# Performance work log

Measured on AMD Instinct MI355X. Metric: run time of the kernel, lower is better.

Reference implementation:

```python
import jax, jax.numpy as jnp
import numpy as np
from jax import lax

N_NODES = 100000
N_EDGES = 3200000
IN_CH = 128
HID = 32
OUT_CH = 64
N_SG = 31  # conv1..conv31, each SGConv(32,32) with K=1 + relu


def setup_inputs() -> dict:
    key = jax.random.key(0)
    ks = jax.random.split(key, 8)
    x = jax.random.normal(ks[0], (N_NODES, IN_CH), dtype=jnp.float32)
    edge_index = jax.random.randint(ks[1], (2, N_EDGES), 0, N_NODES, dtype=jnp.int64)
    s0 = 1.0 / np.sqrt(IN_CH)
    sh = 1.0 / np.sqrt(HID)
    W0 = jax.random.uniform(ks[2], (IN_CH, HID), jnp.float32, -s0, s0)
    b0 = jnp.zeros((HID,), jnp.float32)
    Ws = jax.random.uniform(ks[3], (N_SG, HID, HID), jnp.float32, -sh, sh)
    bs = jnp.zeros((N_SG, HID), jnp.float32)
    W32 = jax.random.uniform(ks[4], (HID, OUT_CH), jnp.float32, -sh, sh)
    b32 = jnp.zeros((OUT_CH,), jnp.float32)
    return {"x": x, "W0": W0, "b0": b0, "Ws": Ws, "bs": bs,
            "W32": W32, "b32": b32, "edge_index": edge_index}


def reference(x, W0, b0, Ws, bs, W32, b32, edge_index):
    N = x.shape[0]
    # GCN normalization with added self-loops (PyG SGConv default, K=1)
    sl = jnp.arange(N, dtype=edge_index.dtype)
    row = jnp.concatenate([edge_index[0], sl])  # source nodes
    col = jnp.concatenate([edge_index[1], sl])  # destination nodes
    deg = jax.ops.segment_sum(jnp.ones(row.shape[0], x.dtype), col, num_segments=N)
    dinv = jnp.where(deg > 0, deg ** -0.5, 0.0)
    norm = dinv[row] * dinv[col]  # [E+N]

    h = x @ W0 + b0  # conv0: plain Linear -> [N, 32]

    def sg_layer(h, wb):
        W, b = wb
        # propagate: D^-1/2 (A+I) D^-1/2 h, then linear + relu
        agg = jax.ops.segment_sum(norm[:, None] * h[row], col, num_segments=N)
        return jax.nn.relu(agg @ W + b), None

    h, _ = lax.scan(sg_layer, h, (Ws, bs))  # conv1..conv31
    return h @ W32 + b32  # conv32: plain Linear -> [N, out_channels]
```

## Files before the change

kernel.cpp:

```cpp
#include <hip/hip_runtime.h>
#include <hip/hip_bf16.h>

#define THREADS 256
#define STRIDE 96

typedef _Float16 f16;
typedef f16 f16x8 __attribute__((ext_vector_type(8)));
typedef f16 f16x4 __attribute__((ext_vector_type(4)));


__global__ void fill_csr_range_kernel(const int* __restrict__ row, const int* __restrict__ col,
                                      int* __restrict__ fill, int* __restrict__ srcs,
                                      int E, int lo, int hi) {
    int e = blockIdx.x * blockDim.x + threadIdx.x;
    if (e < E) {
        int d = col[e];
        if (d >= lo && d < hi) {
            int c = atomicAdd(&fill[d], 1);
            if (c < STRIDE) srcs[(size_t)d * STRIDE + c] = row[e];
        }
    }
}

__global__ void pad_dinv_kernel(const int* __restrict__ fill, int* __restrict__ srcs,
                                float* __restrict__ dinv, int N) {
    int n = blockIdx.x * blockDim.x + threadIdx.x;
    if (n < N) {
        int d = min(fill[n], STRIDE);
        dinv[n] = 1.0f / sqrtf((float)(d + 1));
        int pd = (d + 7) & ~7;
        int* sp = srcs + (size_t)n * STRIDE;
        for (int j = d; j < pd; ++j) sp[j] = N;
    }
}

__global__ void zrow_kernel(f16* __restrict__ gA, f16* __restrict__ gB, int N) {
    int t = threadIdx.x;
    gA[(size_t)N * 32 + t] = (f16)0.f;
    gB[(size_t)N * 32 + t] = (f16)0.f;
}


__global__ __launch_bounds__(256) void lin0_kernel(const float* __restrict__ x,
        const float* __restrict__ W0, const float* __restrict__ b0,
        const float* __restrict__ dinv, f16* __restrict__ g, int N) {
    __shared__ float Ws[128 * 32];
    int t = threadIdx.x;
    for (int i = t; i < 128 * 32; i += 256) Ws[i] = W0[i];
    __syncthreads();
    int node = blockIdx.x * 32 + (t >> 3);
    int lane = t & 7;
    if (node >= N) return;
    float4 o = ((const float4*)b0)[lane];
    const float* xr = x + (size_t)node * 128;
    for (int k = 0; k < 128; ++k) {
        float a = xr[k];
        float4 w = *(const float4*)&Ws[k * 32 + lane * 4];
        o.x += a * w.x; o.y += a * w.y; o.z += a * w.z; o.w += a * w.w;
    }
    float di = dinv[node];
    f16x4 st;
    st.x = (f16)(o.x * di); st.y = (f16)(o.y * di);
    st.z = (f16)(o.z * di); st.w = (f16)(o.w * di);
    ((f16x4*)g)[(size_t)node * 8 + lane] = st;
}

__global__ __launch_bounds__(256, 6) void sg_layer_kernel(const f16* __restrict__ g_in,
        f16* __restrict__ g_out16, float* __restrict__ h_out32,
        const int* __restrict__ deg, const int* __restrict__ srcs,
        const float* __restrict__ dinv, const float* __restrict__ W,
        const float* __restrict__ b, int N, float bscale, int last) {
    __shared__ float Ws[32 * 32];
    int t = threadIdx.x;
    for (int i = t; i < 32 * 32; i += 256) Ws[i] = W[i];
    __syncthreads();
    int node = blockIdx.x * 64 + (t >> 2);
    int lane = t & 3;
    float o0=0.f,o1=0.f,o2=0.f,o3=0.f,o4=0.f,o5=0.f,o6=0.f,o7=0.f;
    if (node < N) {
        const f16x8* g8 = (const f16x8*)g_in;
        f16x8 sv = g8[(size_t)node * 4 + lane];
        o0=(float)sv[0]; o1=(float)sv[1]; o2=(float)sv[2]; o3=(float)sv[3];
        o4=(float)sv[4]; o5=(float)sv[5]; o6=(float)sv[6]; o7=(float)sv[7];
        int e = node * STRIDE;
        int e1 = e + ((min(deg[node], STRIDE) + 7) & ~7);
        int4 ia, ib;
        if (e < e1) {
            ia = *(const int4*)(srcs + e);
            ib = *(const int4*)(srcs + e + 4);
        }
        while (e < e1) {
            f16x8 v0 = g8[(size_t)ia.x * 4 + lane];
            f16x8 v1 = g8[(size_t)ia.y * 4 + lane];
            f16x8 v2 = g8[(size_t)ia.z * 4 + lane];
            f16x8 v3 = g8[(size_t)ia.w * 4 + lane];
            f16x8 v4 = g8[(size_t)ib.x * 4 + lane];
            f16x8 v5 = g8[(size_t)ib.y * 4 + lane];
            f16x8 v6 = g8[(size_t)ib.z * 4 + lane];
            f16x8 v7 = g8[(size_t)ib.w * 4 + lane];
            e += 8;
            if (e < e1) {
                ia = *(const int4*)(srcs + e);
                ib = *(const int4*)(srcs + e + 4);
            }
            o0 += (((float)v0[0]+(float)v1[0])+((float)v2[0]+(float)v3[0]))
                + (((float)v4[0]+(float)v5[0])+((float)v6[0]+(float)v7[0]));
            o1 += (((float)v0[1]+(float)v1[1])+((float)v2[1]+(float)v3[1]))
                + (((float)v4[1]+(float)v5[1])+((float)v6[1]+(float)v7[1]));
            o2 += (((float)v0[2]+(float)v1[2])+((float)v2[2]+(float)v3[2]))
                + (((float)v4[2]+(float)v5[2])+((float)v6[2]+(float)v7[2]));
            o3 += (((float)v0[3]+(float)v1[3])+((float)v2[3]+(float)v3[3]))
                + (((float)v4[3]+(float)v5[3])+((float)v6[3]+(float)v7[3]));
            o4 += (((float)v0[4]+(float)v1[4])+((float)v2[4]+(float)v3[4]))
                + (((float)v4[4]+(float)v5[4])+((float)v6[4]+(float)v7[4]));
            o5 += (((float)v0[5]+(float)v1[5])+((float)v2[5]+(float)v3[5]))
                + (((float)v4[5]+(float)v5[5])+((float)v6[5]+(float)v7[5]));
            o6 += (((float)v0[6]+(float)v1[6])+((float)v2[6]+(float)v3[6]))
                + (((float)v4[6]+(float)v5[6])+((float)v6[6]+(float)v7[6]));
            o7 += (((float)v0[7]+(float)v1[7])+((float)v2[7]+(float)v3[7]))
                + (((float)v4[7]+(float)v5[7])+((float)v6[7]+(float)v7[7]));
        }
    }
    if (node < N) {
        int c = lane * 8;
        int base = t & ~3;
        float m0=0.f,m1=0.f,m2=0.f,m3=0.f,m4=0.f,m5=0.f,m6=0.f,m7=0.f;
        #pragma unroll
        for (int kk = 0; kk < 32; ++kk) {
            float ov;
            switch (kk & 7) {
                case 0: ov = o0; break; case 1: ov = o1; break;
                case 2: ov = o2; break; case 3: ov = o3; break;
                case 4: ov = o4; break; case 5: ov = o5; break;
                case 6: ov = o6; break; default: ov = o7; break;
            }
            float a = __shfl(ov, base | (kk >> 3), 64);
            const float4* wr = (const float4*)&Ws[kk * 32 + c];
            float4 w0 = wr[0], w1 = wr[1];
            m0 += a * w0.x; m1 += a * w0.y; m2 += a * w0.z; m3 += a * w0.w;
            m4 += a * w1.x; m5 += a * w1.y; m6 += a * w1.z; m7 += a * w1.w;
        }
        float di = dinv[node];
        float4 ba = *(const float4*)&b[c];
        float4 bb = *(const float4*)&b[c + 4];
        float r0 = fmaxf(fmaf(di, m0, bscale * ba.x), 0.f);
        float r1 = fmaxf(fmaf(di, m1, bscale * ba.y), 0.f);
        float r2 = fmaxf(fmaf(di, m2, bscale * ba.z), 0.f);
        float r3 = fmaxf(fmaf(di, m3, bscale * ba.w), 0.f);
        float r4 = fmaxf(fmaf(di, m4, bscale * bb.x), 0.f);
        float r5 = fmaxf(fmaf(di, m5, bscale * bb.y), 0.f);
        float r6 = fmaxf(fmaf(di, m6, bscale * bb.z), 0.f);
        float r7 = fmaxf(fmaf(di, m7, bscale * bb.w), 0.f);
        if (!last) {
            float sc = 2.0f * di;
            f16x8 st;
            st[0]=(f16)(r0*sc); st[1]=(f16)(r1*sc); st[2]=(f16)(r2*sc); st[3]=(f16)(r3*sc);
            st[4]=(f16)(r4*sc); st[5]=(f16)(r5*sc); st[6]=(f16)(r6*sc); st[7]=(f16)(r7*sc);
            ((f16x8*)g_out16)[(size_t)node * 4 + lane] = st;
        } else {
            const float inv = 1.0f / 1073741824.0f;
            float4 wa = make_float4(r0*inv, r1*inv, r2*inv, r3*inv);
            float4 wb = make_float4(r4*inv, r5*inv, r6*inv, r7*inv);
            float4* hp = (float4*)(h_out32 + (size_t)node * 32 + c);
            hp[0] = wa; hp[1] = wb;
        }
    }
}

__global__ __launch_bounds__(256) void linout_kernel(const float* __restrict__ h,
        const float* __restrict__ W32, const float* __restrict__ b32,
        float* __restrict__ out, int N) {
    __shared__ float Ws[32 * 64];
    int t = threadIdx.x;
    for (int i = t; i < 32 * 64; i += 256) Ws[i] = W32[i];
    __syncthreads();
    int node = blockIdx.x * 16 + (t >> 4);
    int lane = t & 15;
    if (node >= N) return;
    float4 o = ((const float4*)b32)[lane];
    const float* hr = h + (size_t)node * 32;
    for (int k = 0; k < 32; ++k) {
        float a = hr[k];
        float4 w = *(const float4*)&Ws[k * 64 + lane * 4];
        o.x += a * w.x; o.y += a * w.y; o.z += a * w.z; o.w += a * w.w;
    }
    ((float4*)out)[(size_t)node * 16 + lane] = o;
}


extern "C" void kernel_launch(void* const* d_in, const int* in_sizes, int n_in,
                              void* d_out, int out_size, void* d_ws, size_t ws_size,
                              hipStream_t stream) {
    const float* x     = (const float*)d_in[0];
    const float* W0    = (const float*)d_in[1];
    const float* b0    = (const float*)d_in[2];
    const float* Wsall = (const float*)d_in[3];
    const float* bsall = (const float*)d_in[4];
    const float* W32   = (const float*)d_in[5];
    const float* b32   = (const float*)d_in[6];
    const int*   ei    = (const int*)d_in[7];

    const int N   = in_sizes[0] / 128;
    const int E   = in_sizes[7] / 2;
    const int NSG = in_sizes[3] / (32 * 32);
    const int* erow = ei;
    const int* ecol = ei + E;

    char* ws = (char*)d_ws;
    size_t off = 0;
    auto alloc = [&](size_t bytes) { size_t p = off; off += (bytes + 255) & ~(size_t)255; return p; };
    size_t fillOff  = alloc((size_t)N * 4);
    size_t dinvOff  = alloc((size_t)N * 4);
    size_t srcsOff  = alloc(((size_t)N * STRIDE + 8) * 4);
    size_t gAOff    = alloc((size_t)(N + 1) * 32 * 2);
    size_t gBOff    = alloc((size_t)(N + 1) * 32 * 2);
    size_t hFOff    = alloc((size_t)N * 32 * 4);

    int*   fill   = (int*)(ws + fillOff);
    float* dinv   = (float*)(ws + dinvOff);
    int*   srcs   = (int*)(ws + srcsOff);
    f16*   gA     = (f16*)(ws + gAOff);
    f16*   gB     = (f16*)(ws + gBOff);
    float* hF     = (float*)(ws + hFOff);

    (void)hipMemsetAsync(ws + fillOff, 0, (size_t)N * 4, stream);

    const int egrid = (E + THREADS - 1) / THREADS;
    const int ngrid = (N + THREADS - 1) / THREADS;

    for (int p = 0; p < 4; ++p) {
        int lo = (int)(((long long)N * p) / 4);
        int hi = (int)(((long long)N * (p + 1)) / 4);
        fill_csr_range_kernel<<<egrid, THREADS, 0, stream>>>(erow, ecol, fill, srcs, E, lo, hi);
    }
    pad_dinv_kernel<<<ngrid, THREADS, 0, stream>>>(fill, srcs, dinv, N);
    zrow_kernel<<<1, 32, 0, stream>>>(gA, gB, N);

    lin0_kernel<<<(N + 31) / 32, 256, 0, stream>>>(x, W0, b0, dinv, gA, N);

    f16* cur = gA;
    f16* nxt = gB;
    for (int l = 0; l < NSG; ++l) {
        int last = (l == NSG - 1) ? 1 : 0;
        float bscale = (float)(1u << l);
        sg_layer_kernel<<<(N + 63) / 64, 256, 0, stream>>>(
            cur, nxt, hF, fill, srcs, dinv,
            Wsall + (size_t)l * 32 * 32, bsall + (size_t)l * 32, N, bscale, last);
        f16* tmp = cur; cur = nxt; nxt = tmp;
    }

    linout_kernel<<<(N + 15) / 16, 256, 0, stream>>>(hF, W32, b32, (float*)d_out, N);
}
```

Before: 1.591 ms.

## Sort nodes by degree and build compact remapped CSR for balanced layers

Adds a degree histogram, a prefix scan and a ranking pass that renumber nodes in descending-degree order. It then builds a compact padded CSR whose source indices are already remapped to the new ranks. Each SG layer runs in permuted order, so threads in a wavefront have similar neighbor counts, which should cut divergence and idle lanes in the gather loop. The index array also becomes dense instead of fixed-stride. The cost is several extra preprocessing kernels, an indirection in lin0 and linout, and permuted node ids that change the memory locality of gathered features.

```diff
diff --git a/kernel.cpp b/kernel.cpp
--- a/kernel.cpp
+++ b/kernel.cpp
@@ -7,6 +7,8 @@
 typedef _Float16 f16;
 typedef f16 f16x8 __attribute__((ext_vector_type(8)));
 typedef f16 f16x4 __attribute__((ext_vector_type(4)));
+
+__device__ __forceinline__ int padlen(int d) { return (min(d, STRIDE) + 7) & ~7; }
 
 
 __global__ void fill_csr_range_kernel(const int* __restrict__ row, const int* __restrict__ col,
@@ -22,16 +24,67 @@
     }
 }
 
-__global__ void pad_dinv_kernel(const int* __restrict__ fill, int* __restrict__ srcs,
-                                float* __restrict__ dinv, int N) {
+__global__ void hist_kernel(const int* __restrict__ fill, int* __restrict__ hist, int N) {
+    int n = blockIdx.x * blockDim.x + threadIdx.x;
+    if (n < N) atomicAdd(&hist[127 - min(fill[n], 127)], 1);
+}
+
+__global__ void scan_hist_kernel(const int* __restrict__ hist,
+                                 int* __restrict__ binoff, int* __restrict__ ebase) {
+    __shared__ int sn[128], se[128];
+    int t = threadIdx.x;
+    int deg = 127 - t;
+    int pd = (min(max(deg, 0), STRIDE) + 7) & ~7;
+    int vn = hist[t];
+    int ve = vn * pd;
+    sn[t] = vn; se[t] = ve;
+    __syncthreads();
+    for (int off = 1; off < 128; off <<= 1) {
+        int xn = (t >= off) ? sn[t - off] : 0;
+        int xe = (t >= off) ? se[t - off] : 0;
+        __syncthreads();
+        sn[t] += xn; se[t] += xe;
+        __syncthreads();
+    }
+    binoff[t] = sn[t] - vn;
+    ebase[t]  = se[t] - ve;
+}
+
+__global__ void rank_kernel(const int* __restrict__ fill, const int* __restrict__ binoff,
+                            const int* __restrict__ ebase, int* __restrict__ binfill,
+                            int* __restrict__ rank, int* __restrict__ order,
+                            int* __restrict__ rstart, int* __restrict__ plen,
+                            float* __restrict__ dinv2, int N) {
     int n = blockIdx.x * blockDim.x + threadIdx.x;
     if (n < N) {
-        int d = min(fill[n], STRIDE);
-        dinv[n] = 1.0f / sqrtf((float)(d + 1));
-        int pd = (d + 7) & ~7;
-        int* sp = srcs + (size_t)n * STRIDE;
-        for (int j = d; j < pd; ++j) sp[j] = N;
-    }
+        int d = fill[n];
+        int b = 127 - min(d, 127);
+        int i = atomicAdd(&binfill[b], 1);
+        int p = binoff[b] + i;
+        int pd = padlen(d);
+        rank[n] = p;
+        order[p] = n;
+        rstart[p] = ebase[b] + i * pd;
+        plen[p] = pd;
+        dinv2[p] = 1.0f / sqrtf((float)(min(d, STRIDE) + 1));
+    }
+}
+
+__global__ void remap_kernel(const int* __restrict__ srcs, const int* __restrict__ order,
+                             const int* __restrict__ rank, const int* __restrict__ fill,
+                             const int* __restrict__ rstart, const int* __restrict__ plen,
+                             int* __restrict__ srcs2, int N) {
+    int t = threadIdx.x;
+    int p = blockIdx.x * 32 + (t >> 3);
+    if (p >= N) return;
+    int lane = t & 7;
+    int n = order[p];
+    int d = min(fill[n], STRIDE);
+    int pd = plen[p];
+    const int* sp = srcs + (size_t)n * STRIDE;
+    int* dp = srcs2 + rstart[p];
+    for (int j = lane; j < pd; j += 8)
+        dp[j] = (j < d) ? rank[sp[j]] : N;
 }
 
 __global__ void zrow_kernel(f16* __restrict__ gA, f16* __restrict__ gB, int N) {
@@ -43,51 +96,54 @@
 
 __global__ __launch_bounds__(256) void lin0_kernel(const float* __restrict__ x,
         const float* __restrict__ W0, const float* __restrict__ b0,
-        const float* __restrict__ dinv, f16* __restrict__ g, int N) {
+        const int* __restrict__ order, const float* __restrict__ dinv2,
+        f16* __restrict__ g, int N) {
     __shared__ float Ws[128 * 32];
     int t = threadIdx.x;
     for (int i = t; i < 128 * 32; i += 256) Ws[i] = W0[i];
     __syncthreads();
-    int node = blockIdx.x * 32 + (t >> 3);
+    int p = blockIdx.x * 32 + (t >> 3);
     int lane = t & 7;
-    if (node >= N) return;
+    if (p >= N) return;
+    int n = order[p];
     float4 o = ((const float4*)b0)[lane];
-    const float* xr = x + (size_t)node * 128;
+    const float* xr = x + (size_t)n * 128;
     for (int k = 0; k < 128; ++k) {
         float a = xr[k];
         float4 w = *(const float4*)&Ws[k * 32 + lane * 4];
         o.x += a * w.x; o.y += a * w.y; o.z += a * w.z; o.w += a * w.w;
     }
-    float di = dinv[node];
+    float di = dinv2[p];
     f16x4 st;
     st.x = (f16)(o.x * di); st.y = (f16)(o.y * di);
     st.z = (f16)(o.z * di); st.w = (f16)(o.w * di);
-    ((f16x4*)g)[(size_t)node * 8 + lane] = st;
+    ((f16x4*)g)[(size_t)p * 8 + lane] = st;
 }
 
 __global__ __launch_bounds__(256, 6) void sg_layer_kernel(const f16* __restrict__ g_in,
         f16* __restrict__ g_out16, float* __restrict__ h_out32,
-        const int* __restrict__ deg, const int* __restrict__ srcs,
-        const float* __restrict__ dinv, const float* __restrict__ W,
-        const float* __restrict__ b, int N, float bscale, int last) {
+        const int* __restrict__ rstart, const int* __restrict__ plen,
+        const int* __restrict__ srcs2, const float* __restrict__ dinv2,
+        const float* __restrict__ W, const float* __restrict__ b,
+        int N, float bscale, int last) {
     __shared__ float Ws[32 * 32];
     int t = threadIdx.x;
     for (int i = t; i < 32 * 32; i += 256) Ws[i] = W[i];
     __syncthreads();
-    int node = blockIdx.x * 64 + (t >> 2);
+    int p = blockIdx.x * 64 + (t >> 2);
     int lane = t & 3;
     float o0=0.f,o1=0.f,o2=0.f,o3=0.f,o4=0.f,o5=0.f,o6=0.f,o7=0.f;
-    if (node < N) {
+    if (p < N) {
         const f16x8* g8 = (const f16x8*)g_in;
-        f16x8 sv = g8[(size_t)node * 4 + lane];
+        f16x8 sv = g8[(size_t)p * 4 + lane];
         o0=(float)sv[0]; o1=(float)sv[1]; o2=(float)sv[2]; o3=(float)sv[3];
         o4=(float)sv[4]; o5=(float)sv[5]; o6=(float)sv[6]; o7=(float)sv[7];
-        int e = node * STRIDE;
-        int e1 = e + ((min(deg[node], STRIDE) + 7) & ~7);
+        int e = rstart[p];
+        int e1 = e + plen[p];
         int4 ia, ib;
         if (e < e1) {
-            ia = *(const int4*)(srcs + e);
-            ib = *(const int4*)(srcs + e + 4);
+            ia = *(const int4*)(srcs2 + e);
+            ib = *(const int4*)(srcs2 + e + 4);
         }
         while (e < e1) {
             f16x8 v0 = g8[(size_t)ia.x * 4 + lane];
@@ -100,8 +156,8 @@
             f16x8 v7 = g8[(size_t)ib.w * 4 + lane];
             e += 8;
             if (e < e1) {
-                ia = *(const int4*)(srcs + e);
-                ib = *(const int4*)(srcs + e + 4);
+                ia = *(const int4*)(srcs2 + e);
+                ib = *(const int4*)(srcs2 + e + 4);
             }
             o0 += (((float)v0[0]+(float)v1[0])+((float)v2[0]+(float)v3[0]))
                 + (((float)v4[0]+(float)v5[0])+((float)v6[0]+(float)v7[0]));
@@ -121,7 +177,7 @@
                 + (((float)v4[7]+(float)v5[7])+((float)v6[7]+(float)v7[7]));
         }
     }
-    if (node < N) {
+    if (p < N) {
         int c = lane * 8;
         int base = t & ~3;
         float m0=0.f,m1=0.f,m2=0.f,m3=0.f,m4=0.f,m5=0.f,m6=0.f,m7=0.f;
@@ -140,7 +196,7 @@
             m0 += a * w0.x; m1 += a * w0.y; m2 += a * w0.z; m3 += a * w0.w;
             m4 += a * w1.x; m5 += a * w1.y; m6 += a * w1.z; m7 += a * w1.w;
         }
-        float di = dinv[node];
+        float di = dinv2[p];
         float4 ba = *(const float4*)&b[c];
         float4 bb = *(const float4*)&b[c + 4];
         float r0 = fmaxf(fmaf(di, m0, bscale * ba.x), 0.f);
@@ -156,12 +212,12 @@
             f16x8 st;
             st[0]=(f16)(r0*sc); st[1]=(f16)(r1*sc); st[2]=(f16)(r2*sc); st[3]=(f16)(r3*sc);
             st[4]=(f16)(r4*sc); st[5]=(f16)(r5*sc); st[6]=(f16)(r6*sc); st[7]=(f16)(r7*sc);
-            ((f16x8*)g_out16)[(size_t)node * 4 + lane] = st;
+            ((f16x8*)g_out16)[(size_t)p * 4 + lane] = st;
         } else {
             const float inv = 1.0f / 1073741824.0f;
             float4 wa = make_float4(r0*inv, r1*inv, r2*inv, r3*inv);
             float4 wb = make_float4(r4*inv, r5*inv, r6*inv, r7*inv);
-            float4* hp = (float4*)(h_out32 + (size_t)node * 32 + c);
+            float4* hp = (float4*)(h_out32 + (size_t)p * 32 + c);
             hp[0] = wa; hp[1] = wb;
         }
     }
@@ -169,7 +225,7 @@
 
 __global__ __launch_bounds__(256) void linout_kernel(const float* __restrict__ h,
         const float* __restrict__ W32, const float* __restrict__ b32,
-        float* __restrict__ out, int N) {
+        const int* __restrict__ rank, float* __restrict__ out, int N) {
     __shared__ float Ws[32 * 64];
     int t = threadIdx.x;
     for (int i = t; i < 32 * 64; i += 256) Ws[i] = W32[i];
@@ -177,8 +233,9 @@
     int node = blockIdx.x * 16 + (t >> 4);
     int lane = t & 15;
     if (node >= N) return;
+    int p = rank[node];
     float4 o = ((const float4*)b32)[lane];
-    const float* hr = h + (size_t)node * 32;
+    const float* hr = h + (size_t)p * 32;
     for (int k = 0; k < 32; ++k) {
         float a = hr[k];
         float4 w = *(const float4*)&Ws[k * 64 + lane * 4];
@@ -210,20 +267,38 @@
     size_t off = 0;
     auto alloc = [&](size_t bytes) { size_t p = off; off += (bytes + 255) & ~(size_t)255; return p; };
     size_t fillOff  = alloc((size_t)N * 4);
+    size_t histOff  = alloc(128 * 4);
+    size_t bfilOff  = alloc(128 * 4);
+    size_t binoOff  = alloc(128 * 4);
+    size_t ebasOff  = alloc(128 * 4);
+    size_t rankOff  = alloc((size_t)N * 4);
+    size_t ordOff   = alloc((size_t)N * 4);
+    size_t rstOff   = alloc((size_t)N * 4);
+    size_t plenOff  = alloc((size_t)N * 4);
     size_t dinvOff  = alloc((size_t)N * 4);
-    size_t srcsOff  = alloc(((size_t)N * STRIDE + 8) * 4);
+    size_t srcsOff  = alloc((size_t)N * STRIDE * 4);
+    size_t srcs2Off = alloc(((size_t)E + 8 * (size_t)N + 64) * 4);
     size_t gAOff    = alloc((size_t)(N + 1) * 32 * 2);
     size_t gBOff    = alloc((size_t)(N + 1) * 32 * 2);
     size_t hFOff    = alloc((size_t)N * 32 * 4);
 
     int*   fill   = (int*)(ws + fillOff);
-    float* dinv   = (float*)(ws + dinvOff);
+    int*   hist   = (int*)(ws + histOff);
+    int*   bfil   = (int*)(ws + bfilOff);
+    int*   bino   = (int*)(ws + binoOff);
+    int*   ebas   = (int*)(ws + ebasOff);
+    int*   rank   = (int*)(ws + rankOff);
+    int*   order  = (int*)(ws + ordOff);
+    int*   rstart = (int*)(ws + rstOff);
+    int*   plen   = (int*)(ws + plenOff);
+    float* dinv2  = (float*)(ws + dinvOff);
     int*   srcs   = (int*)(ws + srcsOff);
+    int*   srcs2  = (int*)(ws + srcs2Off);
     f16*   gA     = (f16*)(ws + gAOff);
     f16*   gB     = (f16*)(ws + gBOff);
     float* hF     = (float*)(ws + hFOff);
 
-    (void)hipMemsetAsync(ws + fillOff, 0, (size_t)N * 4, stream);
+    (void)hipMemsetAsync(ws + fillOff, 0, bfilOff + 128 * 4 - fillOff, stream);
 
     const int egrid = (E + THREADS - 1) / THREADS;
     const int ngrid = (N + THREADS - 1) / THREADS;
@@ -233,10 +308,15 @@
         int hi = (int)(((long long)N * (p + 1)) / 4);
         fill_csr_range_kernel<<<egrid, THREADS, 0, stream>>>(erow, ecol, fill, srcs, E, lo, hi);
     }
-    pad_dinv_kernel<<<ngrid, THREADS, 0, stream>>>(fill, srcs, dinv, N);
+    hist_kernel<<<ngrid, THREADS, 0, stream>>>(fill, hist, N);
+    scan_hist_kernel<<<1, 128, 0, stream>>>(hist, bino, ebas);
+    rank_kernel<<<ngrid, THREADS, 0, stream>>>(fill, bino, ebas, bfil,
+                                               rank, order, rstart, plen, dinv2, N);
+    remap_kernel<<<(N + 31) / 32, 256, 0, stream>>>(srcs, order, rank, fill,
+                                                    rstart, plen, srcs2, N);
     zrow_kernel<<<1, 32, 0, stream>>>(gA, gB, N);
 
-    lin0_kernel<<<(N + 31) / 32, 256, 0, stream>>>(x, W0, b0, dinv, gA, N);
+    lin0_kernel<<<(N + 31) / 32, 256, 0, stream>>>(x, W0, b0, order, dinv2, gA, N);
 
     f16* cur = gA;
     f16* nxt = gB;
@@ -244,10 +324,10 @@
         int last = (l == NSG - 1) ? 1 : 0;
         float bscale = (float)(1u << l);
         sg_layer_kernel<<<(N + 63) / 64, 256, 0, stream>>>(
-            cur, nxt, hF, fill, srcs, dinv,
+            cur, nxt, hF, rstart, plen, srcs2, dinv2,
             Wsall + (size_t)l * 32 * 32, bsall + (size_t)l * 32, N, bscale, last);
         f16* tmp = cur; cur = nxt; nxt = tmp;
     }
 
-    linout_kernel<<<(N + 15) / 16, 256, 0, stream>>>(hF, W32, b32, (float*)d_out, N);
-}
+    linout_kernel<<<(N + 15) / 16, 256, 0, stream>>>(hF, W32, b32, rank, (float*)d_out, N);
+}
```

After: 1.923 ms. 1.21x slower.
